# Kernel optimization log

Hardware: AMD Instinct MI355X
Metric: run time of the kernel (lower is better)

The kernel has to match this reference:

```python
import jax, jax.numpy as jnp
import numpy as np

DIN = 1024
DOUT = 1024

def setup_inputs() -> dict:
    key = jax.random.key(0)
    kx, kq, kk, kv = jax.random.split(key, 4)
    x = jax.random.normal(kx, (4, 2048, DIN), dtype=jnp.float32)
    s = 1.0 / np.sqrt(DIN)
    Wq = jax.random.uniform(kq, (DIN, DOUT), dtype=jnp.float32, minval=-s, maxval=s)
    Wk = jax.random.uniform(kk, (DIN, DOUT), dtype=jnp.float32, minval=-s, maxval=s)
    Wv = jax.random.uniform(kv, (DIN, DOUT), dtype=jnp.float32, minval=-s, maxval=s)
    return {"x": x, "Wq": Wq, "Wk": Wk, "Wv": Wv}

def reference(x, Wq, Wk, Wv):
    # q,k,v: [B, T, D]
    q = jnp.einsum('btd,de->bte', x, Wq)
    k = jnp.einsum('btd,de->bte', x, Wk)
    v = jnp.einsum('btd,de->bte', x, Wv)
    # scores: [B, T_q, T_k]; NOTE: no 1/sqrt(d) scaling in original
    scores = jnp.einsum('bqd,bkd->bqk', q, k)
    # Original applies softmax over dim=1 (the QUERY axis), faithfully kept
    weights = jax.nn.softmax(scores, axis=1)
    return jnp.einsum('bqk,bkd->bqd', weights, v)
```

## Files before the change

### kernel.cpp

```cpp
#include <hip/hip_runtime.h>

#define B_   4
#define T_   2048
#define D_   1024
#define MTOK 8192

typedef __attribute__((ext_vector_type(8))) _Float16 half8;
typedef __attribute__((ext_vector_type(4))) float    f32x4;

#define GLD(G, L) __builtin_amdgcn_global_load_lds(                       \
    (const __attribute__((address_space(1))) void*)(G),                   \
    (__attribute__((address_space(3))) void*)(L), 16, 0, 0)

#define BAR()   __builtin_amdgcn_s_barrier()
#define LGKM0() do { asm volatile("s_waitcnt lgkmcnt(0)" ::: "memory");   \
                     __builtin_amdgcn_sched_barrier(0); } while (0)
#define VMW3()  asm volatile("s_waitcnt vmcnt(3)" ::: "memory")
#define VMW2()  asm volatile("s_waitcnt vmcnt(2)" ::: "memory")
#define VMW0()  asm volatile("s_waitcnt vmcnt(0)" ::: "memory")

__device__ __forceinline__ unsigned short f2h(float f) {
  return __builtin_bit_cast(unsigned short, (_Float16)f);
}
__device__ __forceinline__ float h2f(unsigned short u) {
  return (float)__builtin_bit_cast(_Float16, u);
}

__global__ __launch_bounds__(256) void tofp16_kernel(
    const float4* __restrict__ in, ushort4* __restrict__ out, int n4) {
  int i = blockIdx.x * 256 + threadIdx.x;
  if (i >= n4) return;
  float4 v = in[i];
  ushort4 h;
  h.x = f2h(v.x); h.y = f2h(v.y); h.z = f2h(v.z); h.w = f2h(v.w);
  out[i] = h;
}

__global__ __launch_bounds__(256) void wcat_t_kernel(
    const float* __restrict__ Wq, const float* __restrict__ Wk,
    const float* __restrict__ Wv, unsigned short* __restrict__ Wt) {
  __shared__ float tile[32][33];
  int z = blockIdx.z;
  const float* W = (z == 0) ? Wq : ((z == 1) ? Wk : Wv);
  int c0 = blockIdx.x * 32, r0 = blockIdx.y * 32;
  int tx = threadIdx.x & 31, ty = threadIdx.x >> 5;
  #pragma unroll
  for (int i = 0; i < 4; ++i)
    tile[ty + i * 8][tx] = W[(size_t)(r0 + ty + i * 8) * D_ + c0 + tx];
  __syncthreads();
  #pragma unroll
  for (int i = 0; i < 4; ++i) {
    float v = tile[tx][ty + i * 8];
    size_t row = (size_t)z * D_ + c0 + ty + i * 8;
    Wt[row * D_ + r0 + tx] = f2h(v);
  }
}

__global__ __launch_bounds__(256) void vtrans_kernel(
    const unsigned short* __restrict__ QKV, unsigned short* __restrict__ Vt) {
  __shared__ unsigned short tile[64][68];
  int b = blockIdx.z;
  int t0 = blockIdx.x * 64, d0 = blockIdx.y * 64;
  int l16 = threadIdx.x & 15, rr = threadIdx.x >> 4;
  const unsigned short* src =
      QKV + ((size_t)b * 2048 + t0 + rr) * 3072 + 2048 + d0 + l16 * 4;
  #pragma unroll
  for (int i = 0; i < 4; ++i) {
    ushort4 v = *(const ushort4*)(src + (size_t)i * 16 * 3072);
    *(ushort4*)&tile[rr + i * 16][l16 * 4] = v;
  }
  __syncthreads();
  unsigned short* dst = Vt + ((size_t)b * D_ + d0) * 2048 + t0;
  #pragma unroll
  for (int j = 0; j < 4; ++j) {
    int dd = rr + j * 16;
    int tt = l16 * 4;
    ushort4 v;
    v.x = tile[tt + 0][dd]; v.y = tile[tt + 1][dd];
    v.z = tile[tt + 2][dd]; v.w = tile[tt + 3][dd];
    *(ushort4*)(dst + (size_t)dd * 2048 + tt) = v;
  }
}

template <int EPI>
__global__ __launch_bounds__(512, 4) void gemm8p(
    const unsigned short* __restrict__ A, const unsigned short* __restrict__ B,
    void* __restrict__ C0,
    int K, int lda, int ldb, int ldc,
    long aBatch, long bBatch, long cBatch) {
  constexpr int ABY  = 128 * 64;
  constexpr int BUFB = ABY + 16384;
  __shared__ __align__(16) char lds[2 * BUFB];

  const int z = blockIdx.z;
  A += (size_t)z * aBatch;
  B += (size_t)z * bBatch;

  const int nwg = gridDim.x * gridDim.y;
  int s = blockIdx.y * gridDim.x + blockIdx.x;
  s = (s & 7) * (nwg >> 3) + (s >> 3);
  const int bx = s % gridDim.x, by = s / gridDim.x;
  const int brow = by * 128, bcol = bx * 256;

  const int tid = threadIdx.x;
  const int wid = tid >> 6, lane = tid & 63;
  const int wr = wid >> 2, wc = wid & 3;
  const int l15 = lane & 15, g4 = lane >> 4;

  const int scol = ((lane & 3) ^ ((lane >> 3) & 3)) * 8;
  const int srow = lane >> 2;
  int aoff, adst, boffs[2], bdst[2];
  {
    int r0 = wid * 16;
    aoff = (brow + r0 + srow) * lda + scol;
    adst = r0 * 64;
    #pragma unroll
    for (int rg = 0; rg < 2; ++rg) {
      int rb = (wid >> 1) * 64 + rg * 32 + (wid & 1) * 16;
      boffs[rg] = (bcol + rb + srow) * ldb + scol;
      bdst[rg]  = ABY + rb * 64;
    }
  }

  const int rslot = (g4 ^ ((l15 >> 1) & 3)) * 16;
  int aRd[2], bRd[2];
  #pragma unroll
  for (int mh = 0; mh < 2; ++mh) {
    aRd[mh] = (wr * 64 + mh * 32 + l15) * 64 + rslot;
    bRd[mh] = ABY + (wc * 64 + mh * 32 + l15) * 64 + rslot;
  }

#define STAGE_A(bb, tt) \
    GLD(A + (size_t)(aoff + (tt) * 32), lds + (bb) * BUFB + adst)
#define STAGE_B(nh, bb, tt) \
    GLD(B + (size_t)(boffs[nh] + (tt) * 32), lds + (bb) * BUFB + bdst[nh])
#define LOAD_A(mh) do { _Pragma("unroll")                                     \
    for (int mf = 0; mf < 2; ++mf)                                            \
      ar[mf] = *(const half8*)(buf + aRd[mh] + mf * 1024); } while (0)
#define LOAD_B(dst, nh) do { _Pragma("unroll")                                \
    for (int nf = 0; nf < 2; ++nf)                                            \
      dst[nf] = *(const half8*)(buf + bRd[nh] + nf * 1024); } while (0)
#define MFMA_Q(mh, nh, br) do { _Pragma("unroll")                             \
    for (int mf = 0; mf < 2; ++mf) { _Pragma("unroll")                        \
      for (int nf = 0; nf < 2; ++nf) {                                        \
        f32x4& ac = acc[(mh) * 2 + mf][(nh) * 2 + nf];                        \
        ac = __builtin_amdgcn_mfma_f32_16x16x32_f16(ar[mf], br[nf], ac, 0, 0, 0); \
      } } } while (0)

  STAGE_A(0, 0); STAGE_B(0, 0, 0); STAGE_B(1, 0, 0);
  STAGE_A(1, 1); STAGE_B(0, 1, 1); STAGE_B(1, 1, 1);
  VMW3();
  BAR();

  f32x4 acc[4][4] = {};
  half8 ar[2], b0r[2], b1r[2];
  const int nIter = K / 64;

  for (int it = 0; it < nIter; ++it) {
    const bool st = (it + 1 < nIter);
    #pragma unroll
    for (int h = 0; h < 2; ++h) {
      const char* buf = lds + h * BUFB;
      const int tt = 2 * it + 2 + h;
      LOAD_A(0); LOAD_B(b0r, 0);
      BAR(); LGKM0();
      __builtin_amdgcn_s_setprio(1); MFMA_Q(0, 0, b0r);
      __builtin_amdgcn_s_setprio(0); BAR();
      LOAD_B(b1r, 1);
      if (st) STAGE_B(0, h, tt);
      BAR(); LGKM0();
      __builtin_amdgcn_s_setprio(1); MFMA_Q(0, 1, b1r);
      __builtin_amdgcn_s_setprio(0); BAR();
      LOAD_A(1);
      if (st) STAGE_B(1, h, tt);
      BAR(); LGKM0();
      __builtin_amdgcn_s_setprio(1); MFMA_Q(1, 1, b1r);
      __builtin_amdgcn_s_setprio(0); BAR();
      if (st) STAGE_A(h, tt);
      BAR();
      __builtin_amdgcn_s_setprio(1); MFMA_Q(1, 0, b0r);
      __builtin_amdgcn_s_setprio(0);
      if (st) { VMW3(); } else { VMW0(); }
      BAR();
    }
  }

  #pragma unroll
  for (int m = 0; m < 4; ++m) {
    int rowoff = (m >> 1) * 32 + (m & 1) * 16;
    #pragma unroll
    for (int n = 0; n < 4; ++n) {
      int coloff = (n >> 1) * 32 + (n & 1) * 16;
      #pragma unroll
      for (int r = 0; r < 4; ++r) {
        int row = brow + wr * 64 + rowoff + g4 * 4 + r;
        int col = bcol + wc * 64 + coloff + l15;
        float v = acc[m][n][r];
        if constexpr (EPI == 0) {
          float* C = (float*)C0 + (size_t)z * cBatch;
          C[(size_t)row * ldc + col] = v;
        } else {
          unsigned short* C = (unsigned short*)C0 + (size_t)z * cBatch;
          C[(size_t)row * ldc + col] = f2h(v);
        }
      }
    }
  }
#undef STAGE_A
#undef STAGE_B
#undef LOAD_A
#undef LOAD_B
#undef MFMA_Q
}

__global__ __launch_bounds__(512, 2) void gemmPV(
    const unsigned short* __restrict__ Sc, const float* __restrict__ U,
    const unsigned short* __restrict__ Bv, float* __restrict__ out) {
  constexpr int ABY  = 128 * 64;
  constexpr int BUFB = ABY + 16384;
  __shared__ __align__(16) char lds[2 * BUFB];

  const int z = blockIdx.z;
  Sc += (size_t)z * T_ * T_;
  U  += (size_t)z * T_;
  Bv += (size_t)z * D_ * T_;
  float* Co = out + (size_t)z * T_ * D_;

  const int nwg = gridDim.x * gridDim.y;
  int s = blockIdx.y * gridDim.x + blockIdx.x;
  s = (s & 7) * (nwg >> 3) + (s >> 3);
  const int bx = s % gridDim.x, by = s / gridDim.x;
  const int brow = by * 128, bcol = bx * 256;

  const int tid = threadIdx.x;
  const int wid = tid >> 6, lane = tid & 63;
  const int wr = wid >> 2, wc = wid & 3;
  const int l15 = lane & 15, g4 = lane >> 4;

  const int arow = wid * 16 + (lane >> 2);
  const unsigned short* aSrc = Sc + (size_t)(brow + arow) * T_ + (lane & 3) * 8;
  const int awB  = arow * 64 + ((lane & 3) ^ ((lane >> 3) & 3)) * 16;
  const int ucol = (lane & 3) * 8;

  const int scol = ((lane & 3) ^ ((lane >> 3) & 3)) * 8;
  const int srow = lane >> 2;
  int boffs[2], bdst[2];
  #pragma unroll
  for (int rg = 0; rg < 2; ++rg) {
    int rb = (wid >> 1) * 64 + rg * 32 + (wid & 1) * 16;
    boffs[rg] = (bcol + rb + srow) * T_ + scol;
    bdst[rg]  = ABY + rb * 64;
  }

  const int rslot = (g4 ^ ((l15 >> 1) & 3)) * 16;
  int aRd[2], bRd[2];
  #pragma unroll
  for (int mh = 0; mh < 2; ++mh) {
    aRd[mh] = (wr * 64 + mh * 32 + l15) * 64 + rslot;
    bRd[mh] = ABY + (wc * 64 + mh * 32 + l15) * 64 + rslot;
  }

  uint4 rawA;
  float4 uva, uvb;

#define PV_STAGE_B(nh, bb, tt) \
    GLD(Bv + (size_t)(boffs[nh] + (tt) * 32), lds + (bb) * BUFB + bdst[nh])
#define PV_AISSUE(tt) do {                                                    \
    rawA = *(const uint4*)(aSrc + (size_t)(tt) * 32);                         \
    uva  = *(const float4*)(U + (tt) * 32 + ucol);                            \
    uvb  = *(const float4*)(U + (tt) * 32 + ucol + 4); } while (0)
#define PV_AWRITE(bb) do {                                                    \
    const unsigned short* hp = (const unsigned short*)&rawA;                  \
    float uu[8] = {uva.x, uva.y, uva.z, uva.w, uvb.x, uvb.y, uvb.z, uvb.w};   \
    unsigned int w_[4];                                                       \
    _Pragma("unroll") for (int j = 0; j < 4; ++j) {                           \
      float w0 = __expf(h2f(hp[2 * j])     - 64.f) * uu[2 * j];               \
      float w1 = __expf(h2f(hp[2 * j + 1]) - 64.f) * uu[2 * j + 1];           \
      w_[j] = (unsigned int)f2h(w0) | ((unsigned int)f2h(w1) << 16); }        \
    *(uint4*)(lds + (bb) * BUFB + awB) = *(uint4*)w_; } while (0)
#define PV_LOAD_A(mh) do { _Pragma("unroll")                                  \
    for (int mf = 0; mf < 2; ++mf)                                            \
      ar[mf] = *(const half8*)(buf + aRd[mh] + mf * 1024); } while (0)
#define PV_LOAD_B(dst, nh) do { _Pragma("unroll")                             \
    for (int nf = 0; nf < 2; ++nf)                                            \
      dst[nf] = *(const half8*)(buf + bRd[nh] + nf * 1024); } while (0)
#define PV_MFMA(mh, nh, br) do { _Pragma("unroll")                            \
    for (int mf = 0; mf < 2; ++mf) { _Pragma("unroll")                        \
      for (int nf = 0; nf < 2; ++nf) {                                        \
        f32x4& ac = acc[(mh) * 2 + mf][(nh) * 2 + nf];                        \
        ac = __builtin_amdgcn_mfma_f32_16x16x32_f16(ar[mf], br[nf], ac, 0, 0, 0); \
      } } } while (0)

  PV_AISSUE(0);
  PV_STAGE_B(0, 0, 0); PV_STAGE_B(1, 0, 0);
  uint4 rawA1 = *(const uint4*)(aSrc + 32);
  float4 uva1 = *(const float4*)(U + 32 + ucol);
  float4 uvb1 = *(const float4*)(U + 32 + ucol + 4);
  PV_STAGE_B(0, 1, 1); PV_STAGE_B(1, 1, 1);
  VMW2();
  PV_AWRITE(0);
  rawA = rawA1; uva = uva1; uvb = uvb1;
  PV_AWRITE(1);
  asm volatile("s_waitcnt lgkmcnt(0)" ::: "memory");
  BAR();
  VMW0();

  f32x4 acc[4][4] = {};
  half8 ar[2], b0r[2], b1r[2];
  const int NT = T_ / 32;

  for (int it = 0; it < NT / 2; ++it) {
    #pragma unroll
    for (int h = 0; h < 2; ++h) {
      const char* buf = lds + h * BUFB;
      const int tt = 2 * it + 2 + h;
      const bool st = (tt < NT);
      PV_LOAD_A(0); PV_LOAD_B(b0r, 0);
      if (st) PV_AISSUE(tt);
      BAR(); LGKM0();
      __builtin_amdgcn_s_setprio(1); PV_MFMA(0, 0, b0r);
      __builtin_amdgcn_s_setprio(0); BAR();
      PV_LOAD_B(b1r, 1);
      if (st) PV_STAGE_B(0, h, tt);
      BAR(); LGKM0();
      __builtin_amdgcn_s_setprio(1); PV_MFMA(0, 1, b1r);
      __builtin_amdgcn_s_setprio(0); BAR();
      PV_LOAD_A(1);
      if (st) PV_STAGE_B(1, h, tt);
      BAR(); LGKM0();
      __builtin_amdgcn_s_setprio(1); PV_MFMA(1, 1, b1r);
      __builtin_amdgcn_s_setprio(0); BAR();
      if (st) { VMW2(); PV_AWRITE(h); }
      BAR();
      __builtin_amdgcn_s_setprio(1); PV_MFMA(1, 0, b0r);
      __builtin_amdgcn_s_setprio(0);
      if (!st) VMW0();
      BAR();
    }
  }

  #pragma unroll
  for (int m = 0; m < 4; ++m) {
    int rowoff = (m >> 1) * 32 + (m & 1) * 16;
    #pragma unroll
    for (int n = 0; n < 4; ++n) {
      int coloff = (n >> 1) * 32 + (n & 1) * 16;
      #pragma unroll
      for (int r = 0; r < 4; ++r) {
        int row = brow + wr * 64 + rowoff + g4 * 4 + r;
        int col = bcol + wc * 64 + coloff + l15;
        Co[(size_t)row * D_ + col] = acc[m][n][r];
      }
    }
  }
#undef PV_STAGE_B
#undef PV_AISSUE
#undef PV_AWRITE
#undef PV_LOAD_A
#undef PV_LOAD_B
#undef PV_MFMA
}

__global__ __launch_bounds__(256) void sm_sum(const unsigned short* __restrict__ scores,
                                              float* __restrict__ psum) {
  int k = blockIdx.x * 256 + threadIdx.x;
  int qc = blockIdx.y, b = blockIdx.z;
  const unsigned short* S = scores + (size_t)b * T_ * T_ + (size_t)qc * 128 * T_ + k;
  float s = 0.f;
  #pragma unroll 4
  for (int q = 0; q < 128; ++q) s += __expf(h2f(S[(size_t)q * T_]) - 64.0f);
  psum[(b * 16 + qc) * T_ + k] = s;
}

__global__ __launch_bounds__(256) void sm_stats(const float* __restrict__ psum,
                                                float* __restrict__ stats) {
  int i = blockIdx.x * 256 + threadIdx.x;
  int b = i >> 11, k = i & 2047;
  float S = 0.f;
  #pragma unroll
  for (int qc = 0; qc < 16; ++qc) S += psum[(b * 16 + qc) * T_ + k];
  stats[i] = 1.0f / S;
}

extern "C" void kernel_launch(void* const* d_in, const int* in_sizes, int n_in,
                              void* d_out, int out_size, void* d_ws, size_t ws_size,
                              hipStream_t stream) {
  const float* x  = (const float*)d_in[0];
  const float* Wq = (const float*)d_in[1];
  const float* Wk = (const float*)d_in[2];
  const float* Wv = (const float*)d_in[3];
  float* out = (float*)d_out;

  char* ws = (char*)d_ws;
  const size_t MB = 1024ull * 1024ull;
  unsigned short* scoresh = (unsigned short*)(ws);
  unsigned short* QKVh = (unsigned short*)(ws + 32 * MB);
  unsigned short* Vt   = (unsigned short*)(ws + 80 * MB);
  unsigned short* xh   = (unsigned short*)(ws + 96 * MB);
  unsigned short* Wt   = (unsigned short*)(ws + 112 * MB);
  float* psum  = (float*)(ws + 118 * MB);
  float* stats = (float*)(ws + 118 * MB + 512 * 1024);

  tofp16_kernel<<<MTOK * D_ / 4 / 256, 256, 0, stream>>>(
      (const float4*)x, (ushort4*)xh, MTOK * D_ / 4);

  wcat_t_kernel<<<dim3(32, 32, 3), 256, 0, stream>>>(Wq, Wk, Wv, Wt);

  gemm8p<1><<<dim3(3072 / 256, MTOK / 128, 1), 512, 0, stream>>>(
      xh, Wt, QKVh, D_, D_, D_, 3072, 0, 0, 0);

  vtrans_kernel<<<dim3(T_ / 64, D_ / 64, B_), 256, 0, stream>>>(QKVh, Vt);

  gemm8p<1><<<dim3(T_ / 256, T_ / 128, B_), 512, 0, stream>>>(
      QKVh, QKVh + 1024, scoresh, D_, 3072, 3072, T_,
      (long)T_ * 3072, (long)T_ * 3072, (long)T_ * T_);

  sm_sum<<<dim3(8, 16, 4), 256, 0, stream>>>(scoresh, psum);
  sm_stats<<<32, 256, 0, stream>>>(psum, stats);

  gemmPV<<<dim3(D_ / 256, T_ / 128, B_), 512, 0, stream>>>(
      scoresh, stats, Vt, out);
}
```

Before: 212.2 us.

## Fuse softmax column sums into QK^T epilogue and split-K the PV GEMM

The QK^T GEMM epilogue now accumulates exp(score-64) column sums per block and atomically adds them into a global colsum buffer. This removes the separate sm_sum pass that re-read the whole fp16 score matrix. The PV GEMM is split into two K halves across the z grid dimension to double the block count, with results combined by float atomics into an output zeroed by a new kernel. In exchange it adds an extra kernel writing the full output, atomic traffic, and nondeterministic summation order.

```diff
diff --git a/kernel.cpp b/kernel.cpp
--- a/kernel.cpp
+++ b/kernel.cpp
@@ -82,10 +82,20 @@
   }
 }
 
+__global__ __launch_bounds__(256) void zero_kernel(float4* __restrict__ o,
+                                                   int n4,
+                                                   float4* __restrict__ cs,
+                                                   int c4) {
+  int i = blockIdx.x * 256 + threadIdx.x;
+  float4 zz = {0.f, 0.f, 0.f, 0.f};
+  if (i < n4) o[i] = zz;
+  if (i < c4) cs[i] = zz;
+}
+
 template <int EPI>
 __global__ __launch_bounds__(512, 4) void gemm8p(
     const unsigned short* __restrict__ A, const unsigned short* __restrict__ B,
-    void* __restrict__ C0,
+    void* __restrict__ C0, float* __restrict__ CS,
     int K, int lda, int ldb, int ldc,
     long aBatch, long bBatch, long cBatch) {
   constexpr int ABY  = 128 * 64;
@@ -185,24 +195,51 @@
     }
   }
 
-  #pragma unroll
-  for (int m = 0; m < 4; ++m) {
-    int rowoff = (m >> 1) * 32 + (m & 1) * 16;
+  if constexpr (EPI == 1) {
+    unsigned short* C = (unsigned short*)C0 + (size_t)z * cBatch;
+    #pragma unroll
+    for (int m = 0; m < 4; ++m) {
+      int rowoff = (m >> 1) * 32 + (m & 1) * 16;
+      #pragma unroll
+      for (int n = 0; n < 4; ++n) {
+        int coloff = (n >> 1) * 32 + (n & 1) * 16;
+        #pragma unroll
+        for (int r = 0; r < 4; ++r) {
+          int row = brow + wr * 64 + rowoff + g4 * 4 + r;
+          int col = bcol + wc * 64 + coloff + l15;
+          C[(size_t)row * ldc + col] = f2h(acc[m][n][r]);
+        }
+      }
+    }
+  } else {
+    unsigned short* C = (unsigned short*)C0 + (size_t)z * cBatch;
+    float csum[4] = {0.f, 0.f, 0.f, 0.f};
+    #pragma unroll
+    for (int m = 0; m < 4; ++m) {
+      int rowoff = (m >> 1) * 32 + (m & 1) * 16;
+      #pragma unroll
+      for (int n = 0; n < 4; ++n) {
+        int coloff = (n >> 1) * 32 + (n & 1) * 16;
+        #pragma unroll
+        for (int r = 0; r < 4; ++r) {
+          int row = brow + wr * 64 + rowoff + g4 * 4 + r;
+          int col = bcol + wc * 64 + coloff + l15;
+          unsigned short hh = f2h(acc[m][n][r]);
+          C[(size_t)row * ldc + col] = hh;
+          csum[n] += __expf(h2f(hh) - 64.0f);
+        }
+      }
+    }
     #pragma unroll
     for (int n = 0; n < 4; ++n) {
-      int coloff = (n >> 1) * 32 + (n & 1) * 16;
+      csum[n] += __shfl_xor(csum[n], 16);
+      csum[n] += __shfl_xor(csum[n], 32);
+    }
+    if (g4 == 0) {
       #pragma unroll
-      for (int r = 0; r < 4; ++r) {
-        int row = brow + wr * 64 + rowoff + g4 * 4 + r;
-        int col = bcol + wc * 64 + coloff + l15;
-        float v = acc[m][n][r];
-        if constexpr (EPI == 0) {
-          float* C = (float*)C0 + (size_t)z * cBatch;
-          C[(size_t)row * ldc + col] = v;
-        } else {
-          unsigned short* C = (unsigned short*)C0 + (size_t)z * cBatch;
-          C[(size_t)row * ldc + col] = f2h(v);
-        }
+      for (int n = 0; n < 4; ++n) {
+        int col = bcol + wc * 64 + (n >> 1) * 32 + (n & 1) * 16 + l15;
+        unsafeAtomicAdd(CS + (size_t)z * T_ + col, csum[n]);
       }
     }
   }
@@ -220,11 +257,13 @@
   constexpr int BUFB = ABY + 16384;
   __shared__ __align__(16) char lds[2 * BUFB];
 
-  const int z = blockIdx.z;
-  Sc += (size_t)z * T_ * T_;
-  U  += (size_t)z * T_;
-  Bv += (size_t)z * D_ * T_;
-  float* Co = out + (size_t)z * T_ * D_;
+  const int z  = blockIdx.z;
+  const int b  = z >> 1, kh = z & 1;
+  const int k0 = kh * 1024;
+  Sc += (size_t)b * T_ * T_;
+  U  += (size_t)b * T_ + k0;
+  Bv += (size_t)b * D_ * T_;
+  float* Co = out + (size_t)b * T_ * D_;
 
   const int nwg = gridDim.x * gridDim.y;
   int s = blockIdx.y * gridDim.x + blockIdx.x;
@@ -238,7 +277,8 @@
   const int l15 = lane & 15, g4 = lane >> 4;
 
   const int arow = wid * 16 + (lane >> 2);
-  const unsigned short* aSrc = Sc + (size_t)(brow + arow) * T_ + (lane & 3) * 8;
+  const unsigned short* aSrc =
+      Sc + (size_t)(brow + arow) * T_ + k0 + (lane & 3) * 8;
   const int awB  = arow * 64 + ((lane & 3) ^ ((lane >> 3) & 3)) * 16;
   const int ucol = (lane & 3) * 8;
 
@@ -248,7 +288,7 @@
   #pragma unroll
   for (int rg = 0; rg < 2; ++rg) {
     int rb = (wid >> 1) * 64 + rg * 32 + (wid & 1) * 16;
-    boffs[rg] = (bcol + rb + srow) * T_ + scol;
+    boffs[rg] = (bcol + rb + srow) * T_ + k0 + scol;
     bdst[rg]  = ABY + rb * 64;
   }
 
@@ -307,7 +347,7 @@
 
   f32x4 acc[4][4] = {};
   half8 ar[2], b0r[2], b1r[2];
-  const int NT = T_ / 32;
+  const int NT = 1024 / 32;
 
   for (int it = 0; it < NT / 2; ++it) {
     #pragma unroll
@@ -330,7 +370,10 @@
       BAR(); LGKM0();
       __builtin_amdgcn_s_setprio(1); PV_MFMA(1, 1, b1r);
       __builtin_amdgcn_s_setprio(0); BAR();
-      if (st) { VMW2(); PV_AWRITE(h); }
+      if (st) {
+        VMW2(); PV_AWRITE(h);
+        asm volatile("s_waitcnt lgkmcnt(0)" ::: "memory");
+      }
       BAR();
       __builtin_amdgcn_s_setprio(1); PV_MFMA(1, 0, b0r);
       __builtin_amdgcn_s_setprio(0);
@@ -349,7 +392,7 @@
       for (int r = 0; r < 4; ++r) {
         int row = brow + wr * 64 + rowoff + g4 * 4 + r;
         int col = bcol + wc * 64 + coloff + l15;
-        Co[(size_t)row * D_ + col] = acc[m][n][r];
+        unsafeAtomicAdd(&Co[(size_t)row * D_ + col], acc[m][n][r]);
       }
     }
   }
@@ -361,25 +404,10 @@
 #undef PV_MFMA
 }
 
-__global__ __launch_bounds__(256) void sm_sum(const unsigned short* __restrict__ scores,
-                                              float* __restrict__ psum) {
-  int k = blockIdx.x * 256 + threadIdx.x;
-  int qc = blockIdx.y, b = blockIdx.z;
-  const unsigned short* S = scores + (size_t)b * T_ * T_ + (size_t)qc * 128 * T_ + k;
-  float s = 0.f;
-  #pragma unroll 4
-  for (int q = 0; q < 128; ++q) s += __expf(h2f(S[(size_t)q * T_]) - 64.0f);
-  psum[(b * 16 + qc) * T_ + k] = s;
-}
-
-__global__ __launch_bounds__(256) void sm_stats(const float* __restrict__ psum,
+__global__ __launch_bounds__(256) void sm_stats(const float* __restrict__ cs,
                                                 float* __restrict__ stats) {
   int i = blockIdx.x * 256 + threadIdx.x;
-  int b = i >> 11, k = i & 2047;
-  float S = 0.f;
-  #pragma unroll
-  for (int qc = 0; qc < 16; ++qc) S += psum[(b * 16 + qc) * T_ + k];
-  stats[i] = 1.0f / S;
+  stats[i] = 1.0f / cs[i];
 }
 
 extern "C" void kernel_launch(void* const* d_in, const int* in_sizes, int n_in,
@@ -398,8 +426,8 @@
   unsigned short* Vt   = (unsigned short*)(ws + 80 * MB);
   unsigned short* xh   = (unsigned short*)(ws + 96 * MB);
   unsigned short* Wt   = (unsigned short*)(ws + 112 * MB);
-  float* psum  = (float*)(ws + 118 * MB);
-  float* stats = (float*)(ws + 118 * MB + 512 * 1024);
+  float* colsum = (float*)(ws + 118 * MB);
+  float* stats  = (float*)(ws + 118 * MB + 64 * 1024);
 
   tofp16_kernel<<<MTOK * D_ / 4 / 256, 256, 0, stream>>>(
       (const float4*)x, (ushort4*)xh, MTOK * D_ / 4);
@@ -407,17 +435,19 @@
   wcat_t_kernel<<<dim3(32, 32, 3), 256, 0, stream>>>(Wq, Wk, Wv, Wt);
 
   gemm8p<1><<<dim3(3072 / 256, MTOK / 128, 1), 512, 0, stream>>>(
-      xh, Wt, QKVh, D_, D_, D_, 3072, 0, 0, 0);
+      xh, Wt, QKVh, nullptr, D_, D_, D_, 3072, 0, 0, 0);
 
   vtrans_kernel<<<dim3(T_ / 64, D_ / 64, B_), 256, 0, stream>>>(QKVh, Vt);
 
-  gemm8p<1><<<dim3(T_ / 256, T_ / 128, B_), 512, 0, stream>>>(
-      QKVh, QKVh + 1024, scoresh, D_, 3072, 3072, T_,
+  zero_kernel<<<MTOK * D_ / 4 / 256, 256, 0, stream>>>(
+      (float4*)out, MTOK * D_ / 4, (float4*)colsum, B_ * T_ / 4);
+
+  gemm8p<2><<<dim3(T_ / 256, T_ / 128, B_), 512, 0, stream>>>(
+      QKVh, QKVh + 1024, scoresh, colsum, D_, 3072, 3072, T_,
       (long)T_ * 3072, (long)T_ * 3072, (long)T_ * T_);
 
-  sm_sum<<<dim3(8, 16, 4), 256, 0, stream>>>(scoresh, psum);
-  sm_stats<<<32, 256, 0, stream>>>(psum, stats);
-
-  gemmPV<<<dim3(D_ / 256, T_ / 128, B_), 512, 0, stream>>>(
+  sm_stats<<<B_ * T_ / 256, 256, 0, stream>>>(colsum, stats);
+
+  gemmPV<<<dim3(D_ / 256, T_ / 128, 2 * B_), 512, 0, stream>>>(
       scoresh, stats, Vt, out);
 }
```

Result: slower. 228.2 us (+7.6%).
